# Performance work log

Hardware: AMD Instinct MI355X
Metric: run time of the kernel (lower is better)

## Reference

```python
import jax, jax.numpy as jnp
import numpy as np

B, H, W, C = 8, 640, 640, 3
NUM_CLASSES = 80
CONF_THR = 0.05
IOU_THR = 0.5
MAX_DET = 100
BOX_VARIANCE = np.array([0.1, 0.1, 0.2, 0.2], np.float32)
CLASS_OFFSET = 1.0e4  # separates classes in coordinate space -> class-aware NMS


def _make_anchors(h=H, w=W):
    """RetinaNet anchors for levels P3-P7, 9 per location, (cx, cy, w, h)."""
    all_a = []
    for lvl in range(3, 8):
        stride = 2 ** lvl
        fh, fw = h // stride, w // stride
        area = float((2 ** (lvl + 2)) ** 2)  # 32^2 at P3 ... 512^2 at P7
        dims = []
        for ratio in (0.5, 1.0, 2.0):
            ah = np.sqrt(area / ratio)
            aw = area / ah
            for scale in (2 ** 0.0, 2 ** (1.0 / 3.0), 2 ** (2.0 / 3.0)):
                dims.append([aw * scale, ah * scale])
        dims = np.array(dims, np.float32)  # [9, 2]
        cx = (np.arange(fw, dtype=np.float32) + 0.5) * stride
        cy = (np.arange(fh, dtype=np.float32) + 0.5) * stride
        cxg, cyg = np.meshgrid(cx, cy)
        centers = np.broadcast_to(np.stack([cxg, cyg], -1)[:, :, None, :], (fh, fw, 9, 2))
        d = np.broadcast_to(dims[None, None], (fh, fw, 9, 2))
        all_a.append(np.concatenate([centers, d], -1).reshape(-1, 4))
    return np.concatenate(all_a, 0).astype(np.float32)  # [76725, 4]


def setup_inputs() -> dict:
    key = jax.random.key(0)
    k1, k2 = jax.random.split(key)
    images = jax.random.normal(k1, (B, H, W, C), jnp.float32)
    predictions = jax.random.normal(k2, (B, 76725, 4 + NUM_CLASSES), jnp.float32)
    anchor_boxes = jnp.asarray(_make_anchors())
    return {"images": images, "predictions": predictions, "anchor_boxes": anchor_boxes}


def _xywh_to_corners(b):
    cxy, wh = b[..., :2], b[..., 2:]
    return jnp.concatenate([cxy - 0.5 * wh, cxy + 0.5 * wh], -1)


def _iou_one_vs_all(box, boxes):
    # box: [4] corners, boxes: [N, 4] corners
    lt = jnp.maximum(box[:2], boxes[:, :2])
    rb = jnp.minimum(box[2:], boxes[:, 2:])
    wh = jnp.maximum(rb - lt, 0.0)
    inter = wh[:, 0] * wh[:, 1]
    a1 = (box[2] - box[0]) * (box[3] - box[1])
    a2 = (boxes[:, 2] - boxes[:, 0]) * (boxes[:, 3] - boxes[:, 1])
    return inter / (a1 + a2 - inter + 1e-8)


def _nms_single(boxes_xywh, corners_off, classes_f, scores):
    empty_det = jnp.concatenate([jnp.zeros(4, boxes_xywh.dtype),
                                 jnp.array([-1.0, -1.0], boxes_xywh.dtype)])

    def step(s, _):
        idx = jnp.argmax(s)
        sc = s[idx]
        valid = sc > 0.0
        det = jnp.concatenate([boxes_xywh[idx], classes_f[idx][None], sc[None]])
        det = jnp.where(valid, det, empty_det)
        iou = _iou_one_vs_all(corners_off[idx], corners_off)  # [N]
        s = jnp.where((iou > IOU_THR) & valid, -1.0, s)
        s = s.at[idx].set(-1.0)
        return s, det

    _, dets = jax.lax.scan(step, scores, None, length=MAX_DET)
    return dets  # [MAX_DET, 6] = (cx, cy, w, h, class, confidence)


def reference(images, predictions, anchor_boxes):
    box_pred = predictions[:, :, :4]
    cls_prob = jax.nn.sigmoid(predictions[:, :, 4:])
    classes_f = jnp.argmax(cls_prob, axis=-1).astype(box_pred.dtype)  # [B, N]
    conf = jnp.max(cls_prob, axis=-1)                                  # [B, N]
    # decode: offsets scaled by variance, centers relative to anchor wh, sizes via exp
    b = box_pred * jnp.asarray(BOX_VARIANCE)
    a = anchor_boxes[None]  # [1, N, 4]
    boxes = jnp.concatenate([b[..., :2] * a[..., 2:] + a[..., :2],
                             jnp.exp(b[..., 2:]) * a[..., 2:]], -1)     # [B, N, 4] xywh
    corners = _xywh_to_corners(boxes)
    # class offset makes NMS class-aware (per-class suppression)
    corners_off = corners + (classes_f * CLASS_OFFSET)[..., None]
    scores = jnp.where(conf > CONF_THR, conf, -1.0)
    return jax.vmap(_nms_single)(boxes, corners_off, classes_f, scores)  # [B, 100, 6]
```

## Files before the change

### kernel.cpp

```cpp
#include <hip/hip_runtime.h>
#include <math.h>

#define BATCH 8
#define N_ANCH 76725
#define NCLS 80
#define NDET 100
#define NPRED 84
#define NSEG 8
#define SEGCAP 192
#define NSORT 2048
#define CURSOR_STRIDE 16

typedef unsigned long long u64;
typedef unsigned int u32;

__global__ void __launch_bounds__(256) k_decode_scatter(
    const float* __restrict__ pred, const float* __restrict__ anchors,
    int* __restrict__ cursor, float4* __restrict__ bk_c,
    float* __restrict__ bk_s, int* __restrict__ bk_oi) {
#pragma clang fp contract(off)
  int lane = threadIdx.x & 63;
  int wave = threadIdx.x >> 6;
  int g = lane >> 2;
  int p = lane & 3;
  int gid = blockIdx.x * 64 + wave * 16 + g;
  if (gid >= BATCH * N_ANCH) return;
  int b = gid / N_ANCH;
  int i = gid - b * N_ANCH;
  const float4* row = (const float4*)(pred + (size_t)gid * NPRED);

  float l1 = -3.0e38f, l2 = -3.0e38f;
  int i1 = 0, i2 = 0;
#define UPD(LV, IDX)                                          \
  { float l = (LV); int idx = (IDX);                          \
    if (l > l1) { l2 = l1; i2 = i1; l1 = l; i1 = idx; }       \
    else if (l > l2) { l2 = l; i2 = idx; } }

  float4 bp = make_float4(0.f, 0.f, 0.f, 0.f);
  {
    float4 v = row[p];
    if (p == 0) {
      bp = v;
    } else {
      int c0 = p * 4 - 4;
      UPD(v.x, c0) UPD(v.y, c0 + 1) UPD(v.z, c0 + 2) UPD(v.w, c0 + 3)
    }
  }
#pragma unroll
  for (int j = 1; j < 5; ++j) {
    int idx = p + 4 * j;
    float4 v = row[idx];
    int c0 = idx * 4 - 4;
    UPD(v.x, c0) UPD(v.y, c0 + 1) UPD(v.z, c0 + 2) UPD(v.w, c0 + 3)
  }
  if (p == 0) {
    float4 v = row[20];
    UPD(v.x, 76) UPD(v.y, 77) UPD(v.z, 78) UPD(v.w, 79)
  }
#undef UPD

#pragma unroll
  for (int off = 1; off <= 2; off <<= 1) {
    float ol1 = __shfl_xor(l1, off);
    int   oj1 = __shfl_xor(i1, off);
    float ol2 = __shfl_xor(l2, off);
    int   oj2 = __shfl_xor(i2, off);
    bool aW = (l1 > ol1) || (l1 == ol1 && i1 < oj1);
    float w1 = aW ? l1 : ol1;  int wi1 = aW ? i1 : oj1;
    float ca = aW ? l2 : ol2;  int cai = aW ? i2 : oj2;
    float cb = aW ? ol1 : l1;  int cbi = aW ? oj1 : i1;
    bool s2 = (ca > cb) || (ca == cb && cai < cbi);
    l1 = w1; i1 = wi1;
    l2 = s2 ? ca : cb; i2 = s2 ? cai : cbi;
  }

  if (p != 0) return;

  float conf = 1.0f / (1.0f + expf(-l1));
  int cls = i1;
  if (l1 - l2 < 1e-4f) {
    float conf2 = 1.0f / (1.0f + expf(-l2));
    if (conf2 > conf) { conf = conf2; cls = i2; }
    else if (conf2 == conf && i2 < i1) { cls = i2; }
  }
  float score = (conf > 0.05f) ? conf : -1.0f;

  float4 a = *(const float4*)(anchors + (size_t)i * 4);
  float b0 = bp.x * 0.1f, b1 = bp.y * 0.1f, b2 = bp.z * 0.2f, b3 = bp.w * 0.2f;
  float cx = b0 * a.z + a.x;
  float cy = b1 * a.w + a.y;
  float w = expf(b2) * a.z;
  float h = expf(b3) * a.w;
  float offv = (float)cls * 10000.0f;
  float x0 = (cx - 0.5f * w) + offv, y0 = (cy - 0.5f * h) + offv;
  float x1 = (cx + 0.5f * w) + offv, y1 = (cy + 0.5f * h) + offv;

  int bc = b * NCLS + cls;
  int cell = bc * NSEG + (blockIdx.x & (NSEG - 1));
  int slot = atomicAdd(&cursor[cell * CURSOR_STRIDE], 1);
  if (slot < SEGCAP) {
    size_t idxo = (size_t)cell * SEGCAP + slot;
    bk_c[idxo] = make_float4(x0, y0, x1, y1);
    bk_s[idxo] = score;
    bk_oi[idxo] = i;
  }
}

__global__ void __launch_bounds__(256, 1) k_nms_class(
    const int* __restrict__ cursor, const float4* __restrict__ bk_c,
    const float* __restrict__ bk_s, const int* __restrict__ bk_oi,
    u64* __restrict__ keys, int* __restrict__ nsel) {
#pragma clang fp contract(off)
  __shared__ u64 skey[NSORT];
  __shared__ u32 sslot[NSORT];
  __shared__ float4 lc[NSEG * SEGCAP];
  int bc = blockIdx.x;
  int tid = threadIdx.x;

  int cnts[NSEG], offs[NSEG];
  int tot = 0;
#pragma unroll
  for (int s = 0; s < NSEG; ++s) {
    int c = cursor[(bc * NSEG + s) * CURSOR_STRIDE];
    c = (c > SEGCAP) ? SEGCAP : c;
    cnts[s] = c;
    offs[s] = tot;
    tot += c;
  }

#pragma unroll
  for (int s = 0; s < NSEG; ++s) {
    size_t gbase = (size_t)(bc * NSEG + s) * SEGCAP;
    for (int j = tid; j < cnts[s]; j += 256) {
      int dst = offs[s] + j;
      float sc = bk_s[gbase + j];
      u32 o = (u32)bk_oi[gbase + j];
      skey[dst] = (sc > 0.0f)
                      ? (((u64)__float_as_uint(sc) << 32) |
                         (u64)(0xFFFFFFFFu - o))
                      : 0ULL;
      sslot[dst] = (u32)dst;
      lc[dst] = bk_c[gbase + j];
    }
  }
  for (int j = tot + tid; j < NSORT; j += 256) {
    skey[j] = 0ULL;
    sslot[j] = 0u;
  }

  for (int k = 2; k <= NSORT; k <<= 1) {
    for (int j = k >> 1; j > 0; j >>= 1) {
      __syncthreads();
      for (int i = tid; i < NSORT; i += 256) {
        int ixj = i ^ j;
        if (ixj > i) {
          u64 a = skey[i], b = skey[ixj];
          bool desc = ((i & k) == 0);
          bool sw = desc ? (a < b) : (a > b);
          if (sw) {
            skey[i] = b;
            skey[ixj] = a;
            u32 t = sslot[i];
            sslot[i] = sslot[ixj];
            sslot[ixj] = t;
          }
        }
      }
    }
  }
  __syncthreads();
  if (tid >= 64) return;

  int lid = tid;
  float4 accA = make_float4(0.f, 0.f, 0.f, 0.f);
  float4 accB = make_float4(0.f, 0.f, 0.f, 0.f);
  float aA = 0.f, aB = 0.f;
  int na = 0;
  u64* ok = keys + (size_t)bc * NDET;

  for (int idx = 0; idx < NSORT; ++idx) {
    u64 ck = skey[idx];
    if (ck == 0ULL) break;
    float4 q = lc[sslot[idx]];
    float qa = (q.z - q.x) * (q.w - q.y);

    float lxA = fmaxf(accA.x, q.x), lyA = fmaxf(accA.y, q.y);
    float rxA = fminf(accA.z, q.z), ryA = fminf(accA.w, q.w);
    float wA = fmaxf(rxA - lxA, 0.0f), hA = fmaxf(ryA - lyA, 0.0f);
    float inA = wA * hA;
    float iouA = inA / (aA + qa - inA + 1e-8f);

    float lxB = fmaxf(accB.x, q.x), lyB = fmaxf(accB.y, q.y);
    float rxB = fminf(accB.z, q.z), ryB = fminf(accB.w, q.w);
    float wB = fmaxf(rxB - lxB, 0.0f), hB = fmaxf(ryB - lyB, 0.0f);
    float inB = wB * hB;
    float iouB = inB / (aB + qa - inB + 1e-8f);

    bool kill = (iouA > 0.5f) || (iouB > 0.5f);
    if (!__any(kill)) {
      if (lid == 0) ok[na] = ck;
      if (na < 64) {
        if (lid == na) { accA = q; aA = qa; }
      } else {
        if (lid == na - 64) { accB = q; aB = qa; }
      }
      ++na;
      if (na >= NDET) break;
    }
  }
  if (lid == 0) nsel[bc] = na;
}

__device__ __forceinline__ void emit_row(float* __restrict__ out,
                                         const float* __restrict__ pred,
                                         const float* __restrict__ anchors,
                                         int b, int t, u64 key, int cls) {
#pragma clang fp contract(off)
  float* o = out + ((size_t)b * NDET + t) * 6;
  if (key == 0ULL) {
    o[0] = 0.f; o[1] = 0.f; o[2] = 0.f; o[3] = 0.f; o[4] = -1.f; o[5] = -1.f;
    return;
  }
  float scv = __uint_as_float((u32)(key >> 32));
  int oiv = (int)(0xFFFFFFFFu - (u32)key);
  const float* pr = pred + ((size_t)b * N_ANCH + oiv) * NPRED;
  const float* a = anchors + (size_t)oiv * 4;
  float b0 = pr[0] * 0.1f, b1 = pr[1] * 0.1f;
  float b2 = pr[2] * 0.2f, b3 = pr[3] * 0.2f;
  float cx = b0 * a[2] + a[0];
  float cy = b1 * a[3] + a[1];
  float w = expf(b2) * a[2];
  float h = expf(b3) * a[3];
  o[0] = cx; o[1] = cy; o[2] = w; o[3] = h;
  o[4] = (float)cls; o[5] = scv;
}

__global__ void __launch_bounds__(64) k_merge(const u64* __restrict__ keys,
                                              const int* __restrict__ nsel,
                                              const float* __restrict__ pred,
                                              const float* __restrict__ anchors,
                                              float* __restrict__ out) {
  int b = blockIdx.x;
  int lid = threadIdx.x;
  __shared__ u64 lkeys[NCLS * NDET];
  __shared__ int lcnt[NCLS];
  for (int k = lid; k < NCLS; k += 64) {
    int n = nsel[b * NCLS + k];
    lcnt[k] = (n > NDET) ? NDET : n;
  }
  __syncthreads();
  for (int idx = lid; idx < NCLS * NDET; idx += 64) {
    int c = idx / NDET;
    int k = idx - c * NDET;
    lkeys[idx] = (k < lcnt[c]) ? keys[(size_t)(b * NCLS + c) * NDET + k] : 0ULL;
  }
  __syncthreads();

  int cntA = lcnt[lid];
  int cntB = (lid < 16) ? lcnt[64 + lid] : 0;
  int ptrA = 0, ptrB = 0;
  u64 w1 = 0ULL, w2 = 0ULL;
  int w1c = 0, w2c = 0;
  for (int t = 0; t < NDET; ++t) {
    u64 kA = (ptrA < cntA) ? lkeys[lid * NDET + ptrA] : 0ULL;
    u64 kB = (ptrB < cntB) ? lkeys[(64 + lid) * NDET + ptrB] : 0ULL;
    u64 mk; int mc;
    if (kB > kA) { mk = kB; mc = 64 + lid; } else { mk = kA; mc = lid; }
    for (int off = 32; off; off >>= 1) {
      u64 okk = __shfl_xor(mk, off);
      int oc = __shfl_xor(mc, off);
      if (okk > mk) { mk = okk; mc = oc; }
    }
    if (mk == 0ULL) break;
    if (lid == mc) ptrA++;
    if (lid + 64 == mc) ptrB++;
    if (lid == (t & 63)) {
      if (t < 64) { w1 = mk; w1c = mc; } else { w2 = mk; w2c = mc; }
    }
  }
  emit_row(out, pred, anchors, b, lid, w1, w1c);
  if (lid + 64 < NDET) emit_row(out, pred, anchors, b, lid + 64, w2, w2c);
}

extern "C" void kernel_launch(void* const* d_in, const int* in_sizes, int n_in,
                              void* d_out, int out_size, void* d_ws, size_t ws_size,
                              hipStream_t stream) {
  const float* pred = (const float*)d_in[1];
  const float* anchors = (const float*)d_in[2];
  float* out = (float*)d_out;

  const int NBUCK = BATCH * NCLS;
  const size_t SLOTS = (size_t)NBUCK * NSEG * SEGCAP;

  float4* bk_c = (float4*)d_ws;
  u64* keys = (u64*)(bk_c + SLOTS);
  float* bk_s = (float*)(keys + (size_t)NBUCK * NDET);
  int* bk_oi = (int*)(bk_s + SLOTS);
  int* nsel = bk_oi + SLOTS;
  int* cursor = nsel + NBUCK;

  hipMemsetAsync(cursor, 0, (size_t)NBUCK * NSEG * CURSOR_STRIDE * sizeof(int),
                 stream);

  int nb = (BATCH * N_ANCH + 63) / 64;
  k_decode_scatter<<<nb, 256, 0, stream>>>(pred, anchors, cursor, bk_c, bk_s, bk_oi);
  k_nms_class<<<NBUCK, 256, 0, stream>>>(cursor, bk_c, bk_s, bk_oi, keys, nsel);
  k_merge<<<BATCH, 64, 0, stream>>>(keys, nsel, pred, anchors, out);
}
```

Measured before the change: 541.4 us.

## Replace sequential per-candidate NMS scan with winner-broadcast bitmask suppression

The per-class NMS no longer tests each sorted candidate one at a time against all kept boxes. It first gathers the boxes into sorted order in shared memory and precomputes their areas, then keeps a per-lane alive bitmask over 24 chunks. Each step picks the lowest alive index with a wave min-reduction, emits it, and suppresses every overlapping candidate in parallel. This bounds the serial loop to at most 100 iterations instead of one per candidate, at the cost of scanning all live chunks on every step and an extra shared-memory reorder pass.

```diff
diff --git a/kernel.cpp b/kernel.cpp
--- a/kernel.cpp
+++ b/kernel.cpp
@@ -9,6 +9,8 @@
 #define NSEG 8
 #define SEGCAP 192
 #define NSORT 2048
+#define NCAND (NSEG * SEGCAP)
+#define NCHUNK 24
 #define CURSOR_STRIDE 16
 
 typedef unsigned long long u64;
@@ -113,7 +115,8 @@
 #pragma clang fp contract(off)
   __shared__ u64 skey[NSORT];
   __shared__ u32 sslot[NSORT];
-  __shared__ float4 lc[NSEG * SEGCAP];
+  __shared__ float4 lc[NCAND];
+  __shared__ float qa_s[NCAND];
   int bc = blockIdx.x;
   int tid = threadIdx.x;
 
@@ -169,43 +172,61 @@
     }
   }
   __syncthreads();
+
+  float4 rb[NCAND / 256];
+#pragma unroll
+  for (int k = 0; k < NCAND / 256; ++k) {
+    rb[k] = lc[sslot[tid + 256 * k]];
+  }
+  __syncthreads();
+#pragma unroll
+  for (int k = 0; k < NCAND / 256; ++k) {
+    int p = tid + 256 * k;
+    lc[p] = rb[k];
+    qa_s[p] = (rb[k].z - rb[k].x) * (rb[k].w - rb[k].y);
+  }
+  __syncthreads();
   if (tid >= 64) return;
 
   int lid = tid;
-  float4 accA = make_float4(0.f, 0.f, 0.f, 0.f);
-  float4 accB = make_float4(0.f, 0.f, 0.f, 0.f);
-  float aA = 0.f, aB = 0.f;
+  u32 mask = 0;
+#pragma unroll
+  for (int k = 0; k < NCHUNK; ++k) {
+    if (skey[k * 64 + lid] != 0ULL) mask |= (1u << k);
+  }
+
+  u64* ok = keys + (size_t)bc * NDET;
   int na = 0;
-  u64* ok = keys + (size_t)bc * NDET;
-
-  for (int idx = 0; idx < NSORT; ++idx) {
-    u64 ck = skey[idx];
-    if (ck == 0ULL) break;
-    float4 q = lc[sslot[idx]];
-    float qa = (q.z - q.x) * (q.w - q.y);
-
-    float lxA = fmaxf(accA.x, q.x), lyA = fmaxf(accA.y, q.y);
-    float rxA = fminf(accA.z, q.z), ryA = fminf(accA.w, q.w);
-    float wA = fmaxf(rxA - lxA, 0.0f), hA = fmaxf(ryA - lyA, 0.0f);
-    float inA = wA * hA;
-    float iouA = inA / (aA + qa - inA + 1e-8f);
-
-    float lxB = fmaxf(accB.x, q.x), lyB = fmaxf(accB.y, q.y);
-    float rxB = fminf(accB.z, q.z), ryB = fminf(accB.w, q.w);
-    float wB = fmaxf(rxB - lxB, 0.0f), hB = fmaxf(ryB - lyB, 0.0f);
-    float inB = wB * hB;
-    float iouB = inB / (aB + qa - inB + 1e-8f);
-
-    bool kill = (iouA > 0.5f) || (iouB > 0.5f);
-    if (!__any(kill)) {
-      if (lid == 0) ok[na] = ck;
-      if (na < 64) {
-        if (lid == na) { accA = q; aA = qa; }
-      } else {
-        if (lid == na - 64) { accB = q; aB = qa; }
+  for (;;) {
+    int m = __ffs(mask);
+    int p = m ? ((m - 1) * 64 + lid) : 0x7FFFFFFF;
+#pragma unroll
+    for (int off = 32; off; off >>= 1) {
+      int o = __shfl_xor(p, off);
+      p = (o < p) ? o : p;
+    }
+    if (p == 0x7FFFFFFF) break;
+
+    float4 wb = lc[p];
+    float pa = qa_s[p];
+    if (lid == 0) ok[na] = skey[p];
+    ++na;
+    if (na >= NDET) break;
+
+#pragma unroll
+    for (int k = 0; k < NCHUNK; ++k) {
+      if (__any((mask >> k) & 1)) {
+        int cp = k * 64 + lid;
+        float4 q = lc[cp];
+        float qa = qa_s[cp];
+        float lx = fmaxf(wb.x, q.x), ly = fmaxf(wb.y, q.y);
+        float rx = fminf(wb.z, q.z), ry = fminf(wb.w, q.w);
+        float ww = fmaxf(rx - lx, 0.0f), hh = fmaxf(ry - ly, 0.0f);
+        float inter = ww * hh;
+        float iou = inter / (pa + qa - inter + 1e-8f);
+        bool kill = (iou > 0.5f) | (cp == p);
+        mask = kill ? (mask & ~(1u << k)) : mask;
       }
-      ++na;
-      if (na >= NDET) break;
     }
   }
   if (lid == 0) nsel[bc] = na;
```

New measurement: 1.019 ms. 1.88x slower.
